# Kernel optimization log

Hardware: AMD Instinct MI355X
Metric: run time of the kernel (lower is better)

## Reference

```python
import jax, jax.numpy as jnp
import numpy as np

B, S, D, H = 2, 2048, 1024, 16
HW = D // H  # head width = 64


def setup_inputs() -> dict:
    key = jax.random.key(0)
    ks = jax.random.split(key, 9)
    x = jax.random.normal(ks[0], (B, S, D), dtype=jnp.float32)
    mask = jax.random.randint(ks[1], (B, S), 0, 2, dtype=jnp.int32)
    pos = jax.random.normal(ks[2], (B, S, S), dtype=jnp.float32) * 0.02
    wq = jax.random.normal(ks[3], (D, D), dtype=jnp.float32) * 0.02
    bq = jnp.zeros((D,), dtype=jnp.float32)
    wk = jax.random.normal(ks[4], (D, D), dtype=jnp.float32) * 0.02
    bk = jnp.zeros((D,), dtype=jnp.float32)
    wv = jax.random.normal(ks[5], (D, D), dtype=jnp.float32) * 0.02
    bv = jnp.zeros((D,), dtype=jnp.float32)
    return {"x": x, "mask": mask, "pos": pos,
            "wq": wq, "bq": bq, "wk": wk, "bk": bk, "wv": wv, "bv": bv}


def reference(x, mask, pos, wq, bq, wk, bk, wv, bv):
    # QKV projections (torch Linear: y = x @ W^T + b)
    q = (x @ wq.T + bq).reshape(B, S, H, HW)
    k = (x @ wk.T + bk).reshape(B, S, H, HW)
    v = (x @ wv.T + bv).reshape(B, S, H, HW)
    # scores: (B, H, Sq, Sk)
    scores = jnp.einsum('bqhd,bkhd->bhqk', q, k) / jnp.sqrt(jnp.float32(HW))
    scores = scores + pos[:, None, :, :]
    m = mask.astype(jnp.float32)[:, None, None, :]
    scores = scores - 10000.0 * (1.0 - m)
    attn = jax.nn.softmax(scores, axis=-1)  # dropout p=0 (inference)
    h = jnp.einsum('bhqk,bkhd->bqhd', attn, v).reshape(B, S, D)
    return h
```

## Files before the change

kernel.cpp:

```cpp
#include <hip/hip_runtime.h>

#define B_ 2
#define S_ 2048
#define D_ 1024
#define H_ 16
#define HW_ 64
#define NT_ (S_ / 64)

typedef __attribute__((ext_vector_type(8))) short s16x8;
typedef __attribute__((ext_vector_type(4))) float f32x4;
typedef __attribute__((ext_vector_type(2))) unsigned int u32x2;
typedef __attribute__((ext_vector_type(4))) unsigned int u32x4;

__device__ __forceinline__ unsigned short f2bf(float f) {
  unsigned int x = __builtin_bit_cast(unsigned int, f);
  x += 0x7fffu + ((x >> 16) & 1u);
  return (unsigned short)(x >> 16);
}
__device__ __forceinline__ float bf2f(unsigned short u) {
  unsigned int x = ((unsigned int)u) << 16;
  return __builtin_bit_cast(float, x);
}
__device__ __forceinline__ unsigned int cvtpk_bf16(float lo, float hi) {
  unsigned int r;
  asm("v_cvt_pk_bf16_f32 %0, %1, %2" : "=v"(r) : "v"(lo), "v"(hi));
  return r;
}
__device__ __forceinline__ void gload16(const void* g, void* l) {
  __builtin_amdgcn_global_load_lds(
      (const __attribute__((address_space(1))) unsigned int*)g,
      (__attribute__((address_space(3))) unsigned int*)l, 16, 0, 0);
}

__global__ __launch_bounds__(256) void cvt_all(const float* __restrict__ x,
                                               const float* __restrict__ wq,
                                               const float* __restrict__ wk,
                                               const float* __restrict__ wv,
                                               const float* __restrict__ pos,
                                               const int* __restrict__ mask,
                                               unsigned short* __restrict__ xb,
                                               unsigned short* __restrict__ wb,
                                               unsigned short* __restrict__ posb) {
  const int blk = blockIdx.x;
  if (blk < 2048) {
    int i = blk * 256 + threadIdx.x;
    const float4* s = (const float4*)x;
    float4 a = s[2 * i], b = s[2 * i + 1];
    s16x8 o;
    o[0] = (short)f2bf(a.x); o[1] = (short)f2bf(a.y);
    o[2] = (short)f2bf(a.z); o[3] = (short)f2bf(a.w);
    o[4] = (short)f2bf(b.x); o[5] = (short)f2bf(b.y);
    o[6] = (short)f2bf(b.z); o[7] = (short)f2bf(b.w);
    ((s16x8*)xb)[i] = o;
  } else if (blk < 3584) {
    int blk2 = blk - 2048;
    const float* src = (blk2 < 512) ? wq : (blk2 < 1024) ? wk : wv;
    int i = (blk2 & 511) * 256 + threadIdx.x;
    const float4* s = (const float4*)src;
    float4 a = s[2 * i], b = s[2 * i + 1];
    s16x8 o;
    o[0] = (short)f2bf(a.x); o[1] = (short)f2bf(a.y);
    o[2] = (short)f2bf(a.z); o[3] = (short)f2bf(a.w);
    o[4] = (short)f2bf(b.x); o[5] = (short)f2bf(b.y);
    o[6] = (short)f2bf(b.z); o[7] = (short)f2bf(b.w);
    ((s16x8*)wb)[(size_t)(blk2 >> 9) * (D_ * D_ / 8) + i] = o;
  } else {
    int i = (blk - 3584) * 256 + threadIdx.x;
    int e = i * 8;
    int b = e / (S_ * S_);
    int k = e & (S_ - 1);
    const float4* s = (const float4*)pos;
    float4 a = s[2 * i], c = s[2 * i + 1];
    const int* mrow = mask + b * S_ + k;
    const float L2E = 1.4426950408889634f;
    float f[8] = {a.x, a.y, a.z, a.w, c.x, c.y, c.z, c.w};
    s16x8 o;
#pragma unroll
    for (int j = 0; j < 8; ++j) {
      float bias = mrow[j] ? 0.0f : -14427.0f;
      o[j] = (short)f2bf(f[j] * L2E + bias);
    }
    ((s16x8*)posb)[i] = o;
  }
}

__global__ __launch_bounds__(256) void qkv_gemm(const unsigned short* __restrict__ X,
                                                const unsigned short* __restrict__ W3,
                                                const float* __restrict__ bq,
                                                const float* __restrict__ bk,
                                                const float* __restrict__ bv,
                                                unsigned short* __restrict__ O3,
                                                unsigned short* __restrict__ VT) {
  const int mat = blockIdx.z;
  const unsigned short* Wp = W3 + (size_t)mat * (D_ * D_);
  const float* bias = (mat == 0) ? bq : (mat == 1) ? bk : bv;
  unsigned short* Op = O3 + (size_t)mat * ((size_t)B_ * S_ * D_);

  const int bm = blockIdx.y * 128, bn = blockIdx.x * 128;
  const int tid = threadIdx.x;
  const int lane = tid & 63, w = tid >> 6;
  const int wr = (w >> 1) * 64, wc = (w & 1) * 64;
  const int l15 = lane & 15, lh = lane >> 4;

  __shared__ __align__(16) unsigned short Al[128 * 64];
  __shared__ __align__(16) unsigned short Wl[128 * 64];

  f32x4 acc[4][4];
#pragma unroll
  for (int m = 0; m < 4; ++m)
#pragma unroll
    for (int n = 0; n < 4; ++n) acc[m][n] = (f32x4){0.f, 0.f, 0.f, 0.f};

  const int srow = lane >> 3;
  const int scol = ((lane & 7) ^ srow) * 8;
  const int i0 = w * 4;

  for (int k0 = 0; k0 < D_; k0 += 64) {
    __syncthreads();
#pragma unroll
    for (int i2 = 0; i2 < 4; ++i2) {
      int i = i0 + i2;
      int row = 8 * i + srow;
      gload16(X + (size_t)(bm + row) * D_ + k0 + scol, Al + i * 512);
      gload16(Wp + (size_t)(bn + row) * D_ + k0 + scol, Wl + i * 512);
    }
    __syncthreads();
#pragma unroll
    for (int kb = 0; kb < 2; ++kb) {
      const int cs = (kb * 32 + lh * 8) ^ ((l15 & 7) * 8);
      s16x8 af[4], wf[4];
#pragma unroll
      for (int m = 0; m < 4; ++m)
        af[m] = *(const s16x8*)(Al + (wr + m * 16 + l15) * 64 + cs);
#pragma unroll
      for (int n = 0; n < 4; ++n)
        wf[n] = *(const s16x8*)(Wl + (wc + n * 16 + l15) * 64 + cs);
      if (mat == 2) {
#pragma unroll
        for (int m = 0; m < 4; ++m)
#pragma unroll
          for (int n = 0; n < 4; ++n)
            acc[m][n] =
                __builtin_amdgcn_mfma_f32_16x16x32_bf16(wf[n], af[m], acc[m][n], 0, 0, 0);
      } else {
#pragma unroll
        for (int m = 0; m < 4; ++m)
#pragma unroll
          for (int n = 0; n < 4; ++n)
            acc[m][n] =
                __builtin_amdgcn_mfma_f32_16x16x32_bf16(af[m], wf[n], acc[m][n], 0, 0, 0);
      }
    }
  }

  if (mat == 2) {
#pragma unroll
    for (int n = 0; n < 4; ++n) {
      f32x4 b4 = *(const f32x4*)(bias + bn + wc + n * 16 + lh * 4);
#pragma unroll
      for (int m = 0; m < 4; ++m) {
        int t = bm + wr + m * 16 + l15;
        int bb = t >> 11, s = t & (S_ - 1);
#pragma unroll
        for (int r = 0; r < 4; ++r) {
          int f = bn + wc + n * 16 + lh * 4 + r;
          VT[((size_t)(bb * H_ + (f >> 6)) * HW_ + (f & 63)) * S_ + s] =
              f2bf(acc[m][n][r] + b4[r]);
        }
      }
    }
  } else {
    const float oscale = (mat == 0) ? 0.18033688751411092f : 1.0f;
#pragma unroll
    for (int n = 0; n < 4; ++n) {
      int col = bn + wc + n * 16 + l15;
      float bval = bias[col];
#pragma unroll
      for (int m = 0; m < 4; ++m) {
        int row0 = bm + wr + m * 16 + lh * 4;
#pragma unroll
        for (int r = 0; r < 4; ++r)
          Op[(size_t)(row0 + r) * D_ + col] = f2bf((acc[m][n][r] + bval) * oscale);
      }
    }
  }
}

__global__ __launch_bounds__(256, 4) void attn_kernel(
    const unsigned short* __restrict__ Q,
    const unsigned short* __restrict__ K,
    const unsigned short* __restrict__ VT,
    const unsigned short* __restrict__ POSM,
    float* __restrict__ OUT) {
  const int h = blockIdx.x, qt = blockIdx.y, b = blockIdx.z;
  const int tid = threadIdx.x;
  const int lane = tid & 63, w = tid >> 6;
  const int l15 = lane & 15, lh = lane >> 4;
  const int qp = w >> 1, kh = w & 1;

  __shared__ __align__(16) unsigned short Kl[2][64 * 64];
  __shared__ __align__(16) unsigned short Vl[2][64 * 64];

  const int swzk = ((l15 & 3) | (((l15 >> 2) & 1) << 2)) * 8;
  const int swzv = ((l15 & 3) | ((l15 & 8) >> 1)) * 8;
  const int rowbase = kh * 32 + 8 * (l15 >> 2) + (l15 & 3);

  const int srow = lane >> 3;
  const int scol = ((lane & 7) ^ ((lane >> 3) & 3) ^ ((w & 1) << 2)) * 8;
  const unsigned short* Kbase = K + (size_t)b * S_ * D_ + h * HW_;
  const unsigned short* Vbase = VT + ((size_t)(b * H_ + h) * HW_) * S_;

  auto stage = [&](int buf, int kt) {
    const int k0 = kt * 64;
#pragma unroll
    for (int i = 0; i < 2; ++i) {
      const int rb = i * 32 + w * 8;
      gload16(Kbase + (size_t)(k0 + rb + srow) * D_ + scol, &Kl[buf][rb * 64]);
      gload16(Vbase + (size_t)(rb + srow) * S_ + k0 + scol, &Vl[buf][rb * 64]);
    }
  };

  const int q0 = qt * 64 + qp * 32;
  const int qg0 = q0 + l15, qg1 = q0 + 16 + l15;
  const unsigned short* Pp0 = POSM + (size_t)(b * S_ + qg0) * S_ + kh * 32 + lh * 8;
  const unsigned short* Pp1 = POSM + (size_t)(b * S_ + qg1) * S_ + kh * 32 + lh * 8;

  s16x8 pm_c[2], pm_n[2];
  pm_c[0] = *(const s16x8*)(Pp0);
  pm_c[1] = *(const s16x8*)(Pp1);
  stage(0, 0);

  s16x8 qf[2][2];
  {
    const unsigned short* qp0 = Q + (size_t)(b * S_ + qg0) * D_ + h * HW_ + lh * 8;
    const unsigned short* qp1 = Q + (size_t)(b * S_ + qg1) * D_ + h * HW_ + lh * 8;
    qf[0][0] = *(const s16x8*)qp0;
    qf[0][1] = *(const s16x8*)(qp0 + 32);
    qf[1][0] = *(const s16x8*)qp1;
    qf[1][1] = *(const s16x8*)(qp1 + 32);
  }

  f32x4 Oc[2][4];
#pragma unroll
  for (int s = 0; s < 2; ++s)
#pragma unroll
    for (int n = 0; n < 4; ++n) Oc[s][n] = (f32x4){0.f, 0.f, 0.f, 0.f};
  float lsq[2] = {0.f, 0.f};

  for (int kt = 0; kt < NT_; ++kt) {
    const int cur = kt & 1;

    if (kt + 1 < NT_) {
      pm_n[0] = *(const s16x8*)(Pp0 + (kt + 1) * 64);
      pm_n[1] = *(const s16x8*)(Pp1 + (kt + 1) * 64);
      stage(cur ^ 1, kt + 1);
      asm volatile("s_waitcnt vmcnt(6)" ::: "memory");
    } else {
      asm volatile("s_waitcnt vmcnt(0)" ::: "memory");
    }
    asm volatile("s_barrier" ::: "memory");

    const unsigned short* Kc = Kl[cur];
    const unsigned short* Vc = Vl[cur];

    s16x8 kf0[2], kf1[2];
#pragma unroll
    for (int n = 0; n < 2; ++n) {
      const unsigned short* kr = Kc + (rowbase + n * 4) * 64;
      kf0[n] = *(const s16x8*)(kr + ((lh * 8) ^ swzk));
      kf1[n] = *(const s16x8*)(kr + ((32 + lh * 8) ^ swzk));
    }

    f32x4 sc[2][2];
    __builtin_amdgcn_s_setprio(1);
#pragma unroll
    for (int s = 0; s < 2; ++s)
#pragma unroll
      for (int n = 0; n < 2; ++n) {
        f32x4 c;
#pragma unroll
        for (int r = 0; r < 4; ++r)
          c[r] = bf2f((unsigned short)pm_c[s][n * 4 + r]);
        c = __builtin_amdgcn_mfma_f32_16x16x32_bf16(kf0[n], qf[s][0], c, 0, 0, 0);
        c = __builtin_amdgcn_mfma_f32_16x16x32_bf16(kf1[n], qf[s][1], c, 0, 0, 0);
        sc[s][n] = c;
      }
    __builtin_amdgcn_s_setprio(0);

#pragma unroll
    for (int s = 0; s < 2; ++s)
#pragma unroll
      for (int n = 0; n < 2; ++n)
#pragma unroll
        for (int r = 0; r < 4; ++r) {
          float p = __builtin_amdgcn_exp2f(sc[s][n][r]);
          sc[s][n][r] = p;
          lsq[s] += p;
        }

    __builtin_amdgcn_s_setprio(1);
    s16x8 vf[4];
#pragma unroll
    for (int n = 0; n < 4; ++n)
      vf[n] = *(const s16x8*)(Vc + (n * 16 + l15) * 64 + ((kh * 32 + lh * 8) ^ swzv));
#pragma unroll
    for (int s = 0; s < 2; ++s) {
      u32x4 pw;
      pw[0] = cvtpk_bf16(sc[s][0][0], sc[s][0][1]);
      pw[1] = cvtpk_bf16(sc[s][0][2], sc[s][0][3]);
      pw[2] = cvtpk_bf16(sc[s][1][0], sc[s][1][1]);
      pw[3] = cvtpk_bf16(sc[s][1][2], sc[s][1][3]);
      s16x8 pf = __builtin_bit_cast(s16x8, pw);
#pragma unroll
      for (int n = 0; n < 4; ++n)
        Oc[s][n] = __builtin_amdgcn_mfma_f32_16x16x32_bf16(vf[n], pf, Oc[s][n], 0, 0, 0);
    }
    __builtin_amdgcn_s_setprio(0);

    asm volatile("s_barrier" ::: "memory");

    pm_c[0] = pm_n[0];
    pm_c[1] = pm_n[1];
  }

#pragma unroll
  for (int s = 0; s < 2; ++s) {
    lsq[s] += __shfl_xor(lsq[s], 16, 64);
    lsq[s] += __shfl_xor(lsq[s], 32, 64);
  }

  __syncthreads();
  f32x4* xO = (f32x4*)Kl;
  float* xL = (float*)Vl;
  if (kh) {
#pragma unroll
    for (int s = 0; s < 2; ++s) {
#pragma unroll
      for (int n = 0; n < 4; ++n)
        xO[((qp * 2 + s) * 4 + n) * 64 + lane] = Oc[s][n];
      if (lh == 0) xL[(qp * 2 + s) * 16 + l15] = lsq[s];
    }
  }
  __syncthreads();
  if (!kh) {
#pragma unroll
    for (int s = 0; s < 2; ++s) {
      float ltot = lsq[s] + xL[(qp * 2 + s) * 16 + l15];
      float inv = 1.0f / ltot;
      int qg = q0 + s * 16 + l15;
      float* outp = OUT + (size_t)(b * S_ + qg) * D_ + h * HW_ + lh * 4;
#pragma unroll
      for (int n = 0; n < 4; ++n) {
        f32x4 o = xO[((qp * 2 + s) * 4 + n) * 64 + lane];
#pragma unroll
        for (int r = 0; r < 4; ++r) o[r] = (o[r] + Oc[s][n][r]) * inv;
        *(f32x4*)(outp + n * 16) = o;
      }
    }
  }
}

extern "C" void kernel_launch(void* const* d_in, const int* in_sizes, int n_in,
                              void* d_out, int out_size, void* d_ws, size_t ws_size,
                              hipStream_t stream) {
  const float* x   = (const float*)d_in[0];
  const int*   msk = (const int*)d_in[1];
  const float* pos = (const float*)d_in[2];
  const float* wq  = (const float*)d_in[3];
  const float* bq  = (const float*)d_in[4];
  const float* wk  = (const float*)d_in[5];
  const float* bk  = (const float*)d_in[6];
  const float* wv  = (const float*)d_in[7];
  const float* bv  = (const float*)d_in[8];
  float* out = (float*)d_out;

  char* ws = (char*)d_ws;
  unsigned short* xb   = (unsigned short*)(ws);
  unsigned short* wb   = (unsigned short*)(ws + 8388608);
  unsigned short* qkv  = (unsigned short*)(ws + 14680064);
  unsigned short* posb = (unsigned short*)(ws + 31457280);
  unsigned short* vt   = (unsigned short*)(ws + 48234496);

  cvt_all<<<7680, 256, 0, stream>>>(x, wq, wk, wv, pos, msk, xb, wb, posb);

  qkv_gemm<<<dim3(D_ / 128, (B_ * S_) / 128, 3), 256, 0, stream>>>(
      xb, wb, bq, bk, bv, qkv, vt);

  attn_kernel<<<dim3(H_, S_ / 64, B_), 256, 0, stream>>>(
      qkv, qkv + (size_t)B_ * S_ * D_, vt, posb, out);
}
```

Before: 118.6 us.

## Triple-buffer K tiles and prefetch next K fragments into registers

```diff
diff --git a/kernel.cpp b/kernel.cpp
--- a/kernel.cpp
+++ b/kernel.cpp
@@ -9,7 +9,6 @@
 
 typedef __attribute__((ext_vector_type(8))) short s16x8;
 typedef __attribute__((ext_vector_type(4))) float f32x4;
-typedef __attribute__((ext_vector_type(2))) unsigned int u32x2;
 typedef __attribute__((ext_vector_type(4))) unsigned int u32x4;
 
 __device__ __forceinline__ unsigned short f2bf(float f) {
@@ -198,7 +197,7 @@
   const int l15 = lane & 15, lh = lane >> 4;
   const int qp = w >> 1, kh = w & 1;
 
-  __shared__ __align__(16) unsigned short Kl[2][64 * 64];
+  __shared__ __align__(16) unsigned short Kl[3][64 * 64];
   __shared__ __align__(16) unsigned short Vl[2][64 * 64];
 
   const int swzk = ((l15 & 3) | (((l15 >> 2) & 1) << 2)) * 8;
@@ -210,12 +209,19 @@
   const unsigned short* Kbase = K + (size_t)b * S_ * D_ + h * HW_;
   const unsigned short* Vbase = VT + ((size_t)(b * H_ + h) * HW_) * S_;
 
-  auto stage = [&](int buf, int kt) {
+  auto Kst = [&](int buf, int kt) {
     const int k0 = kt * 64;
 #pragma unroll
     for (int i = 0; i < 2; ++i) {
       const int rb = i * 32 + w * 8;
       gload16(Kbase + (size_t)(k0 + rb + srow) * D_ + scol, &Kl[buf][rb * 64]);
+    }
+  };
+  auto Vst = [&](int buf, int kt) {
+    const int k0 = kt * 64;
+#pragma unroll
+    for (int i = 0; i < 2; ++i) {
+      const int rb = i * 32 + w * 8;
       gload16(Vbase + (size_t)(rb + srow) * S_ + k0 + scol, &Vl[buf][rb * 64]);
     }
   };
@@ -225,10 +231,12 @@
   const unsigned short* Pp0 = POSM + (size_t)(b * S_ + qg0) * S_ + kh * 32 + lh * 8;
   const unsigned short* Pp1 = POSM + (size_t)(b * S_ + qg1) * S_ + kh * 32 + lh * 8;
 
-  s16x8 pm_c[2], pm_n[2];
-  pm_c[0] = *(const s16x8*)(Pp0);
-  pm_c[1] = *(const s16x8*)(Pp1);
-  stage(0, 0);
+  s16x8 pm[2][2];
+  Vst(0, 0);
+  pm[0][0] = *(const s16x8*)(Pp0);
+  pm[0][1] = *(const s16x8*)(Pp1);
+  Kst(0, 0);
+  Kst(1, 1);
 
   s16x8 qf[2][2];
   {
@@ -247,28 +255,38 @@
     for (int n = 0; n < 4; ++n) Oc[s][n] = (f32x4){0.f, 0.f, 0.f, 0.f};
   float lsq[2] = {0.f, 0.f};
 
+  s16x8 kf0[2][2], kf1[2][2];
+
+#pragma unroll 2
   for (int kt = 0; kt < NT_; ++kt) {
-    const int cur = kt & 1;
-
-    if (kt + 1 < NT_) {
-      pm_n[0] = *(const s16x8*)(Pp0 + (kt + 1) * 64);
-      pm_n[1] = *(const s16x8*)(Pp1 + (kt + 1) * 64);
-      stage(cur ^ 1, kt + 1);
-      asm volatile("s_waitcnt vmcnt(6)" ::: "memory");
+    const int pc = kt & 1, pn = pc ^ 1;
+
+    if (kt < NT_ - 1) {
+      asm volatile("s_waitcnt vmcnt(2)" ::: "memory");
     } else {
       asm volatile("s_waitcnt vmcnt(0)" ::: "memory");
     }
     asm volatile("s_barrier" ::: "memory");
 
-    const unsigned short* Kc = Kl[cur];
-    const unsigned short* Vc = Vl[cur];
-
-    s16x8 kf0[2], kf1[2];
-#pragma unroll
-    for (int n = 0; n < 2; ++n) {
-      const unsigned short* kr = Kc + (rowbase + n * 4) * 64;
-      kf0[n] = *(const s16x8*)(kr + ((lh * 8) ^ swzk));
-      kf1[n] = *(const s16x8*)(kr + ((32 + lh * 8) ^ swzk));
+    if (kt + 2 < NT_) {
+      Vst(pn, kt + 1);
+      pm[pn][0] = *(const s16x8*)(Pp0 + (kt + 1) * 64);
+      pm[pn][1] = *(const s16x8*)(Pp1 + (kt + 1) * 64);
+      Kst((kt + 2) % 3, kt + 2);
+    } else if (kt + 1 < NT_) {
+      Vst(pn, kt + 1);
+      pm[pn][0] = *(const s16x8*)(Pp0 + (kt + 1) * 64);
+      pm[pn][1] = *(const s16x8*)(Pp1 + (kt + 1) * 64);
+    }
+
+    if (kt == 0) {
+      const unsigned short* Kc = Kl[0];
+#pragma unroll
+      for (int n = 0; n < 2; ++n) {
+        const unsigned short* kr = Kc + (rowbase + n * 4) * 64;
+        kf0[0][n] = *(const s16x8*)(kr + ((lh * 8) ^ swzk));
+        kf1[0][n] = *(const s16x8*)(kr + ((32 + lh * 8) ^ swzk));
+      }
     }
 
     f32x4 sc[2][2];
@@ -280,12 +298,17 @@
         f32x4 c;
 #pragma unroll
         for (int r = 0; r < 4; ++r)
-          c[r] = bf2f((unsigned short)pm_c[s][n * 4 + r]);
-        c = __builtin_amdgcn_mfma_f32_16x16x32_bf16(kf0[n], qf[s][0], c, 0, 0, 0);
-        c = __builtin_amdgcn_mfma_f32_16x16x32_bf16(kf1[n], qf[s][1], c, 0, 0, 0);
+          c[r] = bf2f((unsigned short)pm[pc][s][n * 4 + r]);
+        c = __builtin_amdgcn_mfma_f32_16x16x32_bf16(kf0[pc][n], qf[s][0], c, 0, 0, 0);
+        c = __builtin_amdgcn_mfma_f32_16x16x32_bf16(kf1[pc][n], qf[s][1], c, 0, 0, 0);
         sc[s][n] = c;
       }
     __builtin_amdgcn_s_setprio(0);
+
+    s16x8 vf[4];
+#pragma unroll
+    for (int n = 0; n < 4; ++n)
+      vf[n] = *(const s16x8*)(&Vl[pc][(n * 16 + l15) * 64 + ((kh * 32 + lh * 8) ^ swzv)]);
 
 #pragma unroll
     for (int s = 0; s < 2; ++s)
@@ -299,10 +322,6 @@
         }
 
     __builtin_amdgcn_s_setprio(1);
-    s16x8 vf[4];
-#pragma unroll
-    for (int n = 0; n < 4; ++n)
-      vf[n] = *(const s16x8*)(Vc + (n * 16 + l15) * 64 + ((kh * 32 + lh * 8) ^ swzv));
 #pragma unroll
     for (int s = 0; s < 2; ++s) {
       u32x4 pw;
@@ -317,10 +336,20 @@
     }
     __builtin_amdgcn_s_setprio(0);
 
-    asm volatile("s_barrier" ::: "memory");
-
-    pm_c[0] = pm_n[0];
-    pm_c[1] = pm_n[1];
+    if (kt + 1 < NT_) {
+      if (kt + 2 < NT_) {
+        asm volatile("s_waitcnt vmcnt(6)" ::: "memory");
+      } else {
+        asm volatile("s_waitcnt vmcnt(4)" ::: "memory");
+      }
+      const unsigned short* Kn = Kl[(kt + 1) % 3];
+#pragma unroll
+      for (int n = 0; n < 2; ++n) {
+        const unsigned short* kr = Kn + (rowbase + n * 4) * 64;
+        kf0[pn][n] = *(const s16x8*)(kr + ((lh * 8) ^ swzk));
+        kf1[pn][n] = *(const s16x8*)(kr + ((32 + lh * 8) ^ swzk));
+      }
+    }
   }
 
 #pragma unroll
```

Measured after the change: 273.3 us. +130.3%, slower.

## Read fp32 pos directly in attention and triple-buffer K with early fragment loads

Applied to the files above, without the earlier changes.

```diff
diff --git a/kernel.cpp b/kernel.cpp
--- a/kernel.cpp
+++ b/kernel.cpp
@@ -9,7 +9,6 @@
 
 typedef __attribute__((ext_vector_type(8))) short s16x8;
 typedef __attribute__((ext_vector_type(4))) float f32x4;
-typedef __attribute__((ext_vector_type(2))) unsigned int u32x2;
 typedef __attribute__((ext_vector_type(4))) unsigned int u32x4;
 
 __device__ __forceinline__ unsigned short f2bf(float f) {
@@ -17,10 +16,6 @@
   x += 0x7fffu + ((x >> 16) & 1u);
   return (unsigned short)(x >> 16);
 }
-__device__ __forceinline__ float bf2f(unsigned short u) {
-  unsigned int x = ((unsigned int)u) << 16;
-  return __builtin_bit_cast(float, x);
-}
 __device__ __forceinline__ unsigned int cvtpk_bf16(float lo, float hi) {
   unsigned int r;
   asm("v_cvt_pk_bf16_f32 %0, %1, %2" : "=v"(r) : "v"(lo), "v"(hi));
@@ -36,11 +31,10 @@
                                                const float* __restrict__ wq,
                                                const float* __restrict__ wk,
                                                const float* __restrict__ wv,
-                                               const float* __restrict__ pos,
                                                const int* __restrict__ mask,
                                                unsigned short* __restrict__ xb,
                                                unsigned short* __restrict__ wb,
-                                               unsigned short* __restrict__ posb) {
+                                               float* __restrict__ mbias) {
   const int blk = blockIdx.x;
   if (blk < 2048) {
     int i = blk * 256 + threadIdx.x;
@@ -65,22 +59,12 @@
     o[6] = (short)f2bf(b.z); o[7] = (short)f2bf(b.w);
     ((s16x8*)wb)[(size_t)(blk2 >> 9) * (D_ * D_ / 8) + i] = o;
   } else {
-    int i = (blk - 3584) * 256 + threadIdx.x;
-    int e = i * 8;
-    int b = e / (S_ * S_);
-    int k = e & (S_ - 1);
-    const float4* s = (const float4*)pos;
-    float4 a = s[2 * i], c = s[2 * i + 1];
-    const int* mrow = mask + b * S_ + k;
-    const float L2E = 1.4426950408889634f;
-    float f[8] = {a.x, a.y, a.z, a.w, c.x, c.y, c.z, c.w};
-    s16x8 o;
-#pragma unroll
-    for (int j = 0; j < 8; ++j) {
-      float bias = mrow[j] ? 0.0f : -14427.0f;
-      o[j] = (short)f2bf(f[j] * L2E + bias);
-    }
-    ((s16x8*)posb)[i] = o;
+    int t = threadIdx.x;
+#pragma unroll
+    for (int j = 0; j < 16; ++j) {
+      int idx = t * 16 + j;
+      mbias[idx] = mask[idx] ? 0.0f : -10000.0f;
+    }
   }
 }
 
@@ -170,7 +154,7 @@
       }
     }
   } else {
-    const float oscale = (mat == 0) ? 0.18033688751411092f : 1.0f;
+    const float oscale = (mat == 0) ? 0.125f : 1.0f;
 #pragma unroll
     for (int n = 0; n < 4; ++n) {
       int col = bn + wc + n * 16 + l15;
@@ -190,7 +174,8 @@
     const unsigned short* __restrict__ Q,
     const unsigned short* __restrict__ K,
     const unsigned short* __restrict__ VT,
-    const unsigned short* __restrict__ POSM,
+    const float* __restrict__ POS,
+    const float* __restrict__ MB,
     float* __restrict__ OUT) {
   const int h = blockIdx.x, qt = blockIdx.y, b = blockIdx.z;
   const int tid = threadIdx.x;
@@ -198,7 +183,7 @@
   const int l15 = lane & 15, lh = lane >> 4;
   const int qp = w >> 1, kh = w & 1;
 
-  __shared__ __align__(16) unsigned short Kl[2][64 * 64];
+  __shared__ __align__(16) unsigned short Kl[3][64 * 64];
   __shared__ __align__(16) unsigned short Vl[2][64 * 64];
 
   const int swzk = ((l15 & 3) | (((l15 >> 2) & 1) << 2)) * 8;
@@ -210,25 +195,32 @@
   const unsigned short* Kbase = K + (size_t)b * S_ * D_ + h * HW_;
   const unsigned short* Vbase = VT + ((size_t)(b * H_ + h) * HW_) * S_;
 
-  auto stage = [&](int buf, int kt) {
+  auto Kst = [&](int buf, int kt) {
     const int k0 = kt * 64;
 #pragma unroll
     for (int i = 0; i < 2; ++i) {
       const int rb = i * 32 + w * 8;
       gload16(Kbase + (size_t)(k0 + rb + srow) * D_ + scol, &Kl[buf][rb * 64]);
+    }
+  };
+  auto Vst = [&](int buf, int kt) {
+    const int k0 = kt * 64;
+#pragma unroll
+    for (int i = 0; i < 2; ++i) {
+      const int rb = i * 32 + w * 8;
       gload16(Vbase + (size_t)(rb + srow) * S_ + k0 + scol, &Vl[buf][rb * 64]);
     }
   };
 
   const int q0 = qt * 64 + qp * 32;
   const int qg0 = q0 + l15, qg1 = q0 + 16 + l15;
-  const unsigned short* Pp0 = POSM + (size_t)(b * S_ + qg0) * S_ + kh * 32 + lh * 8;
-  const unsigned short* Pp1 = POSM + (size_t)(b * S_ + qg1) * S_ + kh * 32 + lh * 8;
-
-  s16x8 pm_c[2], pm_n[2];
-  pm_c[0] = *(const s16x8*)(Pp0);
-  pm_c[1] = *(const s16x8*)(Pp1);
-  stage(0, 0);
+  const float* Pp0 = POS + (size_t)(b * S_ + qg0) * S_ + kh * 32 + lh * 8;
+  const float* Pp1 = POS + (size_t)(b * S_ + qg1) * S_ + kh * 32 + lh * 8;
+  const float* MBp = MB + b * S_ + kh * 32 + lh * 8;
+
+  Vst(0, 0);
+  Kst(0, 0);
+  Kst(1, 1);
 
   s16x8 qf[2][2];
   {
@@ -240,6 +232,17 @@
     qf[1][1] = *(const s16x8*)(qp1 + 32);
   }
 
+  asm volatile("s_waitcnt vmcnt(0)" ::: "memory");
+  asm volatile("s_barrier" ::: "memory");
+
+  s16x8 kf0E[2], kf1E[2], kf0O[2], kf1O[2];
+#pragma unroll
+  for (int n = 0; n < 2; ++n) {
+    const unsigned short* kr = Kl[0] + (rowbase + n * 4) * 64;
+    kf0E[n] = *(const s16x8*)(kr + ((lh * 8) ^ swzk));
+    kf1E[n] = *(const s16x8*)(kr + ((32 + lh * 8) ^ swzk));
+  }
+
   f32x4 Oc[2][4];
 #pragma unroll
   for (int s = 0; s < 2; ++s)
@@ -247,81 +250,79 @@
     for (int n = 0; n < 4; ++n) Oc[s][n] = (f32x4){0.f, 0.f, 0.f, 0.f};
   float lsq[2] = {0.f, 0.f};
 
-  for (int kt = 0; kt < NT_; ++kt) {
-    const int cur = kt & 1;
-
-    if (kt + 1 < NT_) {
-      pm_n[0] = *(const s16x8*)(Pp0 + (kt + 1) * 64);
-      pm_n[1] = *(const s16x8*)(Pp1 + (kt + 1) * 64);
-      stage(cur ^ 1, kt + 1);
-      asm volatile("s_waitcnt vmcnt(6)" ::: "memory");
-    } else {
-      asm volatile("s_waitcnt vmcnt(0)" ::: "memory");
-    }
-    asm volatile("s_barrier" ::: "memory");
-
-    const unsigned short* Kc = Kl[cur];
-    const unsigned short* Vc = Vl[cur];
-
-    s16x8 kf0[2], kf1[2];
-#pragma unroll
-    for (int n = 0; n < 2; ++n) {
-      const unsigned short* kr = Kc + (rowbase + n * 4) * 64;
-      kf0[n] = *(const s16x8*)(kr + ((lh * 8) ^ swzk));
-      kf1[n] = *(const s16x8*)(kr + ((32 + lh * 8) ^ swzk));
-    }
-
-    f32x4 sc[2][2];
-    __builtin_amdgcn_s_setprio(1);
-#pragma unroll
-    for (int s = 0; s < 2; ++s)
-#pragma unroll
-      for (int n = 0; n < 2; ++n) {
-        f32x4 c;
-#pragma unroll
-        for (int r = 0; r < 4; ++r)
-          c[r] = bf2f((unsigned short)pm_c[s][n * 4 + r]);
-        c = __builtin_amdgcn_mfma_f32_16x16x32_bf16(kf0[n], qf[s][0], c, 0, 0, 0);
-        c = __builtin_amdgcn_mfma_f32_16x16x32_bf16(kf1[n], qf[s][1], c, 0, 0, 0);
-        sc[s][n] = c;
-      }
-    __builtin_amdgcn_s_setprio(0);
-
-#pragma unroll
-    for (int s = 0; s < 2; ++s)
-#pragma unroll
-      for (int n = 0; n < 2; ++n)
-#pragma unroll
-        for (int r = 0; r < 4; ++r) {
-          float p = __builtin_amdgcn_exp2f(sc[s][n][r]);
-          sc[s][n][r] = p;
-          lsq[s] += p;
-        }
-
-    __builtin_amdgcn_s_setprio(1);
-    s16x8 vf[4];
-#pragma unroll
-    for (int n = 0; n < 4; ++n)
-      vf[n] = *(const s16x8*)(Vc + (n * 16 + l15) * 64 + ((kh * 32 + lh * 8) ^ swzv));
-#pragma unroll
-    for (int s = 0; s < 2; ++s) {
-      u32x4 pw;
-      pw[0] = cvtpk_bf16(sc[s][0][0], sc[s][0][1]);
-      pw[1] = cvtpk_bf16(sc[s][0][2], sc[s][0][3]);
-      pw[2] = cvtpk_bf16(sc[s][1][0], sc[s][1][1]);
-      pw[3] = cvtpk_bf16(sc[s][1][2], sc[s][1][3]);
-      s16x8 pf = __builtin_bit_cast(s16x8, pw);
-#pragma unroll
-      for (int n = 0; n < 4; ++n)
-        Oc[s][n] = __builtin_amdgcn_mfma_f32_16x16x32_bf16(vf[n], pf, Oc[s][n], 0, 0, 0);
-    }
-    __builtin_amdgcn_s_setprio(0);
-
-    asm volatile("s_barrier" ::: "memory");
-
-    pm_c[0] = pm_n[0];
-    pm_c[1] = pm_n[1];
-  }
+  const float L2E = 1.4426950408889634f;
+
+#define TILE_BODY(KT, KF0C, KF1C, KF0N, KF1N, CURV)                              \
+  {                                                                              \
+    const int kt_ = (KT);                                                        \
+    asm volatile("s_waitcnt vmcnt(0)" ::: "memory");                             \
+    asm volatile("s_barrier" ::: "memory");                                      \
+    if (kt_ + 1 < NT_) Vst((CURV) ^ 1, kt_ + 1);                                 \
+    if (kt_ + 2 < NT_) Kst((kt_ + 2) % 3, kt_ + 2);                              \
+    f32x4 ps00 = *(const f32x4*)(Pp0 + kt_ * 64);                                \
+    f32x4 ps01 = *(const f32x4*)(Pp0 + kt_ * 64 + 4);                            \
+    f32x4 ps10 = *(const f32x4*)(Pp1 + kt_ * 64);                                \
+    f32x4 ps11 = *(const f32x4*)(Pp1 + kt_ * 64 + 4);                            \
+    f32x4 mb0 = *(const f32x4*)(MBp + kt_ * 64);                                 \
+    f32x4 mb1 = *(const f32x4*)(MBp + kt_ * 64 + 4);                             \
+    f32x4 sc[2][2];                                                              \
+    __builtin_amdgcn_s_setprio(1);                                               \
+    sc[0][0] = __builtin_amdgcn_mfma_f32_16x16x32_bf16(                          \
+        KF1C[0], qf[0][1],                                                       \
+        __builtin_amdgcn_mfma_f32_16x16x32_bf16(KF0C[0], qf[0][0], ps00 + mb0,   \
+                                                0, 0, 0), 0, 0, 0);              \
+    sc[0][1] = __builtin_amdgcn_mfma_f32_16x16x32_bf16(                          \
+        KF1C[1], qf[0][1],                                                       \
+        __builtin_amdgcn_mfma_f32_16x16x32_bf16(KF0C[1], qf[0][0], ps01 + mb1,   \
+                                                0, 0, 0), 0, 0, 0);              \
+    sc[1][0] = __builtin_amdgcn_mfma_f32_16x16x32_bf16(                          \
+        KF1C[0], qf[1][1],                                                       \
+        __builtin_amdgcn_mfma_f32_16x16x32_bf16(KF0C[0], qf[1][0], ps10 + mb0,   \
+                                                0, 0, 0), 0, 0, 0);              \
+    sc[1][1] = __builtin_amdgcn_mfma_f32_16x16x32_bf16(                          \
+        KF1C[1], qf[1][1],                                                       \
+        __builtin_amdgcn_mfma_f32_16x16x32_bf16(KF0C[1], qf[1][0], ps11 + mb1,   \
+                                                0, 0, 0), 0, 0, 0);              \
+    __builtin_amdgcn_s_setprio(0);                                               \
+    s16x8 vf[4];                                                                 \
+    _Pragma("unroll") for (int n = 0; n < 4; ++n)                                \
+        vf[n] = *(const s16x8*)(&Vl[CURV][(n * 16 + l15) * 64 +                  \
+                                          ((kh * 32 + lh * 8) ^ swzv)]);         \
+    if (kt_ + 1 < NT_) {                                                         \
+      const unsigned short* Kn = Kl[(kt_ + 1) % 3];                              \
+      _Pragma("unroll") for (int n = 0; n < 2; ++n) {                            \
+        const unsigned short* kr = Kn + (rowbase + n * 4) * 64;                  \
+        KF0N[n] = *(const s16x8*)(kr + ((lh * 8) ^ swzk));                       \
+        KF1N[n] = *(const s16x8*)(kr + ((32 + lh * 8) ^ swzk));                  \
+      }                                                                          \
+    }                                                                            \
+    _Pragma("unroll") for (int s = 0; s < 2; ++s)                                \
+    _Pragma("unroll") for (int n = 0; n < 2; ++n)                                \
+    _Pragma("unroll") for (int r = 0; r < 4; ++r) {                              \
+      float p = __builtin_amdgcn_exp2f(sc[s][n][r] * L2E);                       \
+      sc[s][n][r] = p;                                                           \
+      lsq[s] += p;                                                               \
+    }                                                                            \
+    __builtin_amdgcn_s_setprio(1);                                               \
+    _Pragma("unroll") for (int s = 0; s < 2; ++s) {                              \
+      u32x4 pw;                                                                  \
+      pw[0] = cvtpk_bf16(sc[s][0][0], sc[s][0][1]);                              \
+      pw[1] = cvtpk_bf16(sc[s][0][2], sc[s][0][3]);                              \
+      pw[2] = cvtpk_bf16(sc[s][1][0], sc[s][1][1]);                              \
+      pw[3] = cvtpk_bf16(sc[s][1][2], sc[s][1][3]);                              \
+      s16x8 pf = __builtin_bit_cast(s16x8, pw);                                  \
+      _Pragma("unroll") for (int n = 0; n < 4; ++n)                              \
+          Oc[s][n] = __builtin_amdgcn_mfma_f32_16x16x32_bf16(vf[n], pf,          \
+                                                             Oc[s][n], 0, 0, 0); \
+    }                                                                            \
+    __builtin_amdgcn_s_setprio(0);                                               \
+  }
+
+  for (int kt2 = 0; kt2 < NT_; kt2 += 2) {
+    TILE_BODY(kt2, kf0E, kf1E, kf0O, kf1O, 0)
+    TILE_BODY(kt2 + 1, kf0O, kf1O, kf0E, kf1E, 1)
+  }
+#undef TILE_BODY
 
 #pragma unroll
   for (int s = 0; s < 2; ++s) {
@@ -378,14 +379,14 @@
   unsigned short* xb   = (unsigned short*)(ws);
   unsigned short* wb   = (unsigned short*)(ws + 8388608);
   unsigned short* qkv  = (unsigned short*)(ws + 14680064);
-  unsigned short* posb = (unsigned short*)(ws + 31457280);
-  unsigned short* vt   = (unsigned short*)(ws + 48234496);
-
-  cvt_all<<<7680, 256, 0, stream>>>(x, wq, wk, wv, pos, msk, xb, wb, posb);
+  unsigned short* vt   = (unsigned short*)(ws + 31457280);
+  float*          mb   = (float*)(ws + 39845888);
+
+  cvt_all<<<3585, 256, 0, stream>>>(x, wq, wk, wv, msk, xb, wb, mb);
 
   qkv_gemm<<<dim3(D_ / 128, (B_ * S_) / 128, 3), 256, 0, stream>>>(
       xb, wb, bq, bk, bv, qkv, vt);
 
   attn_kernel<<<dim3(H_, S_ / 64, B_), 256, 0, stream>>>(
-      qkv, qkv + (size_t)B_ * S_ * D_, vt, posb, out);
-}
+      qkv, qkv + (size_t)B_ * S_ * D_, vt, pos, mb, out);
+}
```

New measurement: 292.0 us. 2.46x slower.

## Read fp32 pos directly in attention and drop the bf16 pos pre-pass

Applied to the files above, without the earlier changes.

```diff
diff --git a/kernel.cpp b/kernel.cpp
--- a/kernel.cpp
+++ b/kernel.cpp
@@ -9,7 +9,6 @@
 
 typedef __attribute__((ext_vector_type(8))) short s16x8;
 typedef __attribute__((ext_vector_type(4))) float f32x4;
-typedef __attribute__((ext_vector_type(2))) unsigned int u32x2;
 typedef __attribute__((ext_vector_type(4))) unsigned int u32x4;
 
 __device__ __forceinline__ unsigned short f2bf(float f) {
@@ -17,10 +16,6 @@
   x += 0x7fffu + ((x >> 16) & 1u);
   return (unsigned short)(x >> 16);
 }
-__device__ __forceinline__ float bf2f(unsigned short u) {
-  unsigned int x = ((unsigned int)u) << 16;
-  return __builtin_bit_cast(float, x);
-}
 __device__ __forceinline__ unsigned int cvtpk_bf16(float lo, float hi) {
   unsigned int r;
   asm("v_cvt_pk_bf16_f32 %0, %1, %2" : "=v"(r) : "v"(lo), "v"(hi));
@@ -36,11 +31,10 @@
                                                const float* __restrict__ wq,
                                                const float* __restrict__ wk,
                                                const float* __restrict__ wv,
-                                               const float* __restrict__ pos,
                                                const int* __restrict__ mask,
                                                unsigned short* __restrict__ xb,
                                                unsigned short* __restrict__ wb,
-                                               unsigned short* __restrict__ posb) {
+                                               float* __restrict__ mbias) {
   const int blk = blockIdx.x;
   if (blk < 2048) {
     int i = blk * 256 + threadIdx.x;
@@ -65,22 +59,12 @@
     o[6] = (short)f2bf(b.z); o[7] = (short)f2bf(b.w);
     ((s16x8*)wb)[(size_t)(blk2 >> 9) * (D_ * D_ / 8) + i] = o;
   } else {
-    int i = (blk - 3584) * 256 + threadIdx.x;
-    int e = i * 8;
-    int b = e / (S_ * S_);
-    int k = e & (S_ - 1);
-    const float4* s = (const float4*)pos;
-    float4 a = s[2 * i], c = s[2 * i + 1];
-    const int* mrow = mask + b * S_ + k;
-    const float L2E = 1.4426950408889634f;
-    float f[8] = {a.x, a.y, a.z, a.w, c.x, c.y, c.z, c.w};
-    s16x8 o;
-#pragma unroll
-    for (int j = 0; j < 8; ++j) {
-      float bias = mrow[j] ? 0.0f : -14427.0f;
-      o[j] = (short)f2bf(f[j] * L2E + bias);
-    }
-    ((s16x8*)posb)[i] = o;
+    int t = threadIdx.x;
+#pragma unroll
+    for (int j = 0; j < 16; ++j) {
+      int idx = t * 16 + j;
+      mbias[idx] = mask[idx] ? 0.0f : -10000.0f;
+    }
   }
 }
 
@@ -170,7 +154,7 @@
       }
     }
   } else {
-    const float oscale = (mat == 0) ? 0.18033688751411092f : 1.0f;
+    const float oscale = (mat == 0) ? 0.125f : 1.0f;
 #pragma unroll
     for (int n = 0; n < 4; ++n) {
       int col = bn + wc + n * 16 + l15;
@@ -190,7 +174,8 @@
     const unsigned short* __restrict__ Q,
     const unsigned short* __restrict__ K,
     const unsigned short* __restrict__ VT,
-    const unsigned short* __restrict__ POSM,
+    const float* __restrict__ POS,
+    const float* __restrict__ MB,
     float* __restrict__ OUT) {
   const int h = blockIdx.x, qt = blockIdx.y, b = blockIdx.z;
   const int tid = threadIdx.x;
@@ -222,12 +207,10 @@
 
   const int q0 = qt * 64 + qp * 32;
   const int qg0 = q0 + l15, qg1 = q0 + 16 + l15;
-  const unsigned short* Pp0 = POSM + (size_t)(b * S_ + qg0) * S_ + kh * 32 + lh * 8;
-  const unsigned short* Pp1 = POSM + (size_t)(b * S_ + qg1) * S_ + kh * 32 + lh * 8;
-
-  s16x8 pm_c[2], pm_n[2];
-  pm_c[0] = *(const s16x8*)(Pp0);
-  pm_c[1] = *(const s16x8*)(Pp1);
+  const float* Pp0 = POS + (size_t)(b * S_ + qg0) * S_ + kh * 32 + lh * 8;
+  const float* Pp1 = POS + (size_t)(b * S_ + qg1) * S_ + kh * 32 + lh * 8;
+  const float* MBp = MB + b * S_ + kh * 32 + lh * 8;
+
   stage(0, 0);
 
   s16x8 qf[2][2];
@@ -240,6 +223,15 @@
     qf[1][1] = *(const s16x8*)(qp1 + 32);
   }
 
+  f32x4 ps_c0, ps_c1, ps_c2, ps_c3, mb_c0, mb_c1;
+  f32x4 ps_n0, ps_n1, ps_n2, ps_n3, mb_n0, mb_n1;
+  ps_c0 = *(const f32x4*)(Pp0);
+  ps_c1 = *(const f32x4*)(Pp0 + 4);
+  ps_c2 = *(const f32x4*)(Pp1);
+  ps_c3 = *(const f32x4*)(Pp1 + 4);
+  mb_c0 = *(const f32x4*)(MBp);
+  mb_c1 = *(const f32x4*)(MBp + 4);
+
   f32x4 Oc[2][4];
 #pragma unroll
   for (int s = 0; s < 2; ++s)
@@ -247,18 +239,23 @@
     for (int n = 0; n < 4; ++n) Oc[s][n] = (f32x4){0.f, 0.f, 0.f, 0.f};
   float lsq[2] = {0.f, 0.f};
 
+  const float L2E = 1.4426950408889634f;
+
   for (int kt = 0; kt < NT_; ++kt) {
     const int cur = kt & 1;
 
+    asm volatile("s_waitcnt vmcnt(6)" ::: "memory");
+    asm volatile("s_barrier" ::: "memory");
+
     if (kt + 1 < NT_) {
-      pm_n[0] = *(const s16x8*)(Pp0 + (kt + 1) * 64);
-      pm_n[1] = *(const s16x8*)(Pp1 + (kt + 1) * 64);
       stage(cur ^ 1, kt + 1);
-      asm volatile("s_waitcnt vmcnt(6)" ::: "memory");
-    } else {
-      asm volatile("s_waitcnt vmcnt(0)" ::: "memory");
-    }
-    asm volatile("s_barrier" ::: "memory");
+      ps_n0 = *(const f32x4*)(Pp0 + (kt + 1) * 64);
+      ps_n1 = *(const f32x4*)(Pp0 + (kt + 1) * 64 + 4);
+      ps_n2 = *(const f32x4*)(Pp1 + (kt + 1) * 64);
+      ps_n3 = *(const f32x4*)(Pp1 + (kt + 1) * 64 + 4);
+      mb_n0 = *(const f32x4*)(MBp + (kt + 1) * 64);
+      mb_n1 = *(const f32x4*)(MBp + (kt + 1) * 64 + 4);
+    }
 
     const unsigned short* Kc = Kl[cur];
     const unsigned short* Vc = Vl[cur];
@@ -273,36 +270,39 @@
 
     f32x4 sc[2][2];
     __builtin_amdgcn_s_setprio(1);
+    {
+      f32x4 c00 = ps_c0 + mb_c0;
+      f32x4 c01 = ps_c1 + mb_c1;
+      f32x4 c10 = ps_c2 + mb_c0;
+      f32x4 c11 = ps_c3 + mb_c1;
+      c00 = __builtin_amdgcn_mfma_f32_16x16x32_bf16(kf0[0], qf[0][0], c00, 0, 0, 0);
+      c01 = __builtin_amdgcn_mfma_f32_16x16x32_bf16(kf0[1], qf[0][0], c01, 0, 0, 0);
+      c10 = __builtin_amdgcn_mfma_f32_16x16x32_bf16(kf0[0], qf[1][0], c10, 0, 0, 0);
+      c11 = __builtin_amdgcn_mfma_f32_16x16x32_bf16(kf0[1], qf[1][0], c11, 0, 0, 0);
+      sc[0][0] = __builtin_amdgcn_mfma_f32_16x16x32_bf16(kf1[0], qf[0][1], c00, 0, 0, 0);
+      sc[0][1] = __builtin_amdgcn_mfma_f32_16x16x32_bf16(kf1[1], qf[0][1], c01, 0, 0, 0);
+      sc[1][0] = __builtin_amdgcn_mfma_f32_16x16x32_bf16(kf1[0], qf[1][1], c10, 0, 0, 0);
+      sc[1][1] = __builtin_amdgcn_mfma_f32_16x16x32_bf16(kf1[1], qf[1][1], c11, 0, 0, 0);
+    }
+    __builtin_amdgcn_s_setprio(0);
+
+    s16x8 vf[4];
+#pragma unroll
+    for (int n = 0; n < 4; ++n)
+      vf[n] = *(const s16x8*)(Vc + (n * 16 + l15) * 64 + ((kh * 32 + lh * 8) ^ swzv));
+
 #pragma unroll
     for (int s = 0; s < 2; ++s)
 #pragma unroll
-      for (int n = 0; n < 2; ++n) {
-        f32x4 c;
-#pragma unroll
-        for (int r = 0; r < 4; ++r)
-          c[r] = bf2f((unsigned short)pm_c[s][n * 4 + r]);
-        c = __builtin_amdgcn_mfma_f32_16x16x32_bf16(kf0[n], qf[s][0], c, 0, 0, 0);
-        c = __builtin_amdgcn_mfma_f32_16x16x32_bf16(kf1[n], qf[s][1], c, 0, 0, 0);
-        sc[s][n] = c;
-      }
-    __builtin_amdgcn_s_setprio(0);
-
-#pragma unroll
-    for (int s = 0; s < 2; ++s)
-#pragma unroll
       for (int n = 0; n < 2; ++n)
 #pragma unroll
         for (int r = 0; r < 4; ++r) {
-          float p = __builtin_amdgcn_exp2f(sc[s][n][r]);
+          float p = __builtin_amdgcn_exp2f(sc[s][n][r] * L2E);
           sc[s][n][r] = p;
           lsq[s] += p;
         }
 
     __builtin_amdgcn_s_setprio(1);
-    s16x8 vf[4];
-#pragma unroll
-    for (int n = 0; n < 4; ++n)
-      vf[n] = *(const s16x8*)(Vc + (n * 16 + l15) * 64 + ((kh * 32 + lh * 8) ^ swzv));
 #pragma unroll
     for (int s = 0; s < 2; ++s) {
       u32x4 pw;
@@ -317,10 +317,8 @@
     }
     __builtin_amdgcn_s_setprio(0);
 
-    asm volatile("s_barrier" ::: "memory");
-
-    pm_c[0] = pm_n[0];
-    pm_c[1] = pm_n[1];
+    ps_c0 = ps_n0; ps_c1 = ps_n1; ps_c2 = ps_n2; ps_c3 = ps_n3;
+    mb_c0 = mb_n0; mb_c1 = mb_n1;
   }
 
 #pragma unroll
@@ -378,14 +376,14 @@
   unsigned short* xb   = (unsigned short*)(ws);
   unsigned short* wb   = (unsigned short*)(ws + 8388608);
   unsigned short* qkv  = (unsigned short*)(ws + 14680064);
-  unsigned short* posb = (unsigned short*)(ws + 31457280);
-  unsigned short* vt   = (unsigned short*)(ws + 48234496);
-
-  cvt_all<<<7680, 256, 0, stream>>>(x, wq, wk, wv, pos, msk, xb, wb, posb);
+  unsigned short* vt   = (unsigned short*)(ws + 31457280);
+  float*          mb   = (float*)(ws + 39845888);
+
+  cvt_all<<<3585, 256, 0, stream>>>(x, wq, wk, wv, msk, xb, wb, mb);
 
   qkv_gemm<<<dim3(D_ / 128, (B_ * S_) / 128, 3), 256, 0, stream>>>(
       xb, wb, bq, bk, bv, qkv, vt);
 
   attn_kernel<<<dim3(H_, S_ / 64, B_), 256, 0, stream>>>(
-      qkv, qkv + (size_t)B_ * S_ * D_, vt, posb, out);
-}
+      qkv, qkv + (size_t)B_ * S_ * D_, vt, pos, mb, out);
+}
```

Result: slower. 172.3 us (+45.2%).
